# Kernel tuning notes

Hardware: AMD Instinct MI355X
Metric: run time of the kernel (lower is better)

The kernel has to match this reference:

```python
import jax, jax.numpy as jnp
import numpy as np

N = 2_097_152          # sampled points
H = 16                 # hash heads / levels
F = 2                  # features per head
M = 524_288            # 2**19 table size
HID = 64               # mlp width
OUT = 3


def setup_inputs() -> dict:
    key = jax.random.key(0)
    ks = jax.random.split(key, 12)
    idx = jax.random.randint(ks[0], (N, H), 0, M, dtype=jnp.int64)
    tables = jax.random.normal(ks[1], (H, M, F), dtype=jnp.float32) * 0.02
    d_in = H * F  # 32
    def lin(k, d1, d2):
        kw, kb = jax.random.split(k)
        s = 1.0 / np.sqrt(d1)
        W = jax.random.uniform(kw, (d1, d2), jnp.float32, -s, s)
        b = jax.random.uniform(kb, (d2,), jnp.float32, -s, s)
        return W, b
    W1, b1 = lin(ks[2], d_in, HID)
    W2, b2 = lin(ks[3], HID, HID)
    W3, b3 = lin(ks[4], HID, HID)
    W4, b4 = lin(ks[5], HID, OUT)
    return {"idx": idx, "tables": tables,
            "W1": W1, "b1": b1, "W2": W2, "b2": b2,
            "W3": W3, "b3": b3, "W4": W4, "b4": b4}


def reference(idx, tables, W1, b1, W2, b2, W3, b3, W4, b4):
    # per-head gather: tables[h][idx[:, h]] -> [N, H, F], then concat heads
    gather = jax.vmap(lambda t, i: t[i], in_axes=(0, 1), out_axes=1)
    x = gather(tables, idx).reshape(idx.shape[0], -1)  # [N, H*F]
    x = jax.nn.relu(x @ W1 + b1)
    x = jax.nn.relu(x @ W2 + b2)
    x = jax.nn.relu(x @ W3 + b3)
    return x @ W4 + b4  # [N, 3]
```

## Files before the change

kernel.cpp:

```cpp
#include <hip/hip_runtime.h>
#include <hip/hip_bf16.h>

typedef __attribute__((ext_vector_type(8))) short short8;
typedef __attribute__((ext_vector_type(4))) float floatx4;
typedef __attribute__((ext_vector_type(4))) int int4v;
typedef __attribute__((ext_vector_type(4))) unsigned int uint4v;

#define MTBL 524288
#define HSTRIDE 72

union U4S8 { uint4v u; short8 s; };

static __device__ __forceinline__ unsigned int pack2bf(float a, float b) {
    union { float f; unsigned int u; } x, y;
    x.f = a; y.f = b;
    unsigned int lo = (x.u + 0x8000u) >> 16;
    unsigned int hi = (y.u + 0x8000u) & 0xFFFF0000u;
    return lo | hi;
}
static __device__ __forceinline__ short bf1(float a) {
    union { float f; unsigned int u; } x;
    x.f = a;
    return (short)((x.u + 0x8000u) >> 16);
}

__global__ __launch_bounds__(256) void ngp_compress(
    const floatx4* __restrict__ tab4, unsigned int* __restrict__ tblC)
{
    const int t = blockIdx.x * 256 + threadIdx.x;
    floatx4 a = __builtin_nontemporal_load(tab4 + (size_t)2 * t);
    floatx4 b = __builtin_nontemporal_load(tab4 + (size_t)2 * t + 1);
    uint4v w;
    w[0] = pack2bf(a[0], a[1]);
    w[1] = pack2bf(a[2], a[3]);
    w[2] = pack2bf(b[0], b[1]);
    w[3] = pack2bf(b[2], b[3]);
    __builtin_nontemporal_store(w, (uint4v*)(tblC + (size_t)4 * t));
}

__global__ __launch_bounds__(256) void ngp_transpose(
    const int* __restrict__ idx, int* __restrict__ idxT, int N)
{
    const int t  = blockIdx.x * 256 + threadIdx.x;
    const int p0 = t * 4;
    const int4v* rows = (const int4v*)idx;
    int4v r[4][4];
#pragma unroll
    for (int p = 0; p < 4; ++p)
#pragma unroll
        for (int c = 0; c < 4; ++c)
            r[p][c] = __builtin_nontemporal_load(rows + (size_t)(p0 + p) * 4 + c);
#pragma unroll
    for (int c = 0; c < 4; ++c)
#pragma unroll
        for (int k = 0; k < 4; ++k) {
            const int h = c * 4 + k;
            int4v w;
            w[0] = r[0][c][k]; w[1] = r[1][c][k]; w[2] = r[2][c][k]; w[3] = r[3][c][k];
            __builtin_nontemporal_store(w, (int4v*)(idxT + (size_t)h * N + p0));
        }
}

__global__ __launch_bounds__(256) void ngp_gather_ph(
    const int* __restrict__ idxT, const unsigned int* __restrict__ tblC,
    unsigned int* __restrict__ xU, int N, int phase, int iters)
{
    const int h    = ((blockIdx.x & 7) << 1) | phase;
    const int slot = blockIdx.x >> 3;
    const int* __restrict__ ih = idxT + (size_t)h * N;
    const unsigned int* __restrict__ th = tblC + (size_t)h * MTBL;
    unsigned int* __restrict__ xh = xU + (size_t)h * N;

    int p = slot * (N >> 8) + (threadIdx.x << 3);
    int4v iv0 = __builtin_nontemporal_load((const int4v*)(ih + p));
    int4v iv1 = __builtin_nontemporal_load((const int4v*)(ih + p + 4));
    for (int it = 0; it < iters; ++it) {
        int4v nv0, nv1;
        if (it + 1 < iters) {
            nv0 = __builtin_nontemporal_load((const int4v*)(ih + p + 2048));
            nv1 = __builtin_nontemporal_load((const int4v*)(ih + p + 2052));
        }
        uint4v w0, w1;
        w0[0] = th[iv0[0]]; w0[1] = th[iv0[1]]; w0[2] = th[iv0[2]]; w0[3] = th[iv0[3]];
        w1[0] = th[iv1[0]]; w1[1] = th[iv1[1]]; w1[2] = th[iv1[2]]; w1[3] = th[iv1[3]];
        __builtin_nontemporal_store(w0, (uint4v*)(xh + p));
        __builtin_nontemporal_store(w1, (uint4v*)(xh + p + 4));
        iv0 = nv0; iv1 = nv1;
        p += 2048;
    }
}

__global__ __launch_bounds__(256, 2) void ngp_mlp(
    const unsigned int* __restrict__ xU,
    const float* __restrict__ W1, const float* __restrict__ b1,
    const float* __restrict__ W2, const float* __restrict__ b2,
    const float* __restrict__ W3, const float* __restrict__ b3,
    const float* __restrict__ W4, const float* __restrict__ b4,
    float* __restrict__ out, int N, int tiles_per_wave)
{
    __shared__ float sW[6144];
    __shared__ __hip_bfloat16 sH[4][16 * HSTRIDE];

    const int tid  = threadIdx.x;
    const int wave = tid >> 6;
    const int lane = tid & 63;
    const int q = lane >> 4;
    const int m = lane & 15;

    short8 A1[4], A2[4][2], A3[4][2], A4[2];
    floatx4 C1[4], C2[4], C3[4], C4;

    for (int i = tid; i < 2048; i += 256) sW[i] = W1[i];
    for (int i = tid; i < 4096; i += 256) sW[2048 + i] = W2[i];
    __syncthreads();
#pragma unroll
    for (int t = 0; t < 4; ++t) {
        short8 a;
#pragma unroll
        for (int j = 0; j < 8; ++j)
            a[j] = bf1(sW[(q * 8 + j) * 64 + t * 16 + m]);
        A1[t] = a;
    }
#pragma unroll
    for (int t = 0; t < 4; ++t)
#pragma unroll
        for (int c = 0; c < 2; ++c) {
            short8 a;
#pragma unroll
            for (int j = 0; j < 8; ++j)
                a[j] = bf1(sW[2048 + (c * 32 + q * 8 + j) * 64 + t * 16 + m]);
            A2[t][c] = a;
        }
    __syncthreads();

    for (int i = tid; i < 4096; i += 256) sW[i] = W3[i];
    if (tid < 192) sW[4096 + tid] = W4[tid];
    if (tid < 64)       sW[4288 + tid] = b1[tid];
    else if (tid < 128) sW[4288 + tid] = b2[tid - 64];
    else if (tid < 192) sW[4288 + tid] = b3[tid - 128];
    else if (tid < 195) sW[4288 + tid] = b4[tid - 192];
    __syncthreads();
#pragma unroll
    for (int t = 0; t < 4; ++t)
#pragma unroll
        for (int c = 0; c < 2; ++c) {
            short8 a;
#pragma unroll
            for (int j = 0; j < 8; ++j)
                a[j] = bf1(sW[(c * 32 + q * 8 + j) * 64 + t * 16 + m]);
            A3[t][c] = a;
        }
#pragma unroll
    for (int c = 0; c < 2; ++c) {
        short8 a;
#pragma unroll
        for (int j = 0; j < 8; ++j)
            a[j] = (m < 3) ? bf1(sW[4096 + (c * 32 + q * 8 + j) * 3 + m]) : (short)0;
        A4[c] = a;
    }
#pragma unroll
    for (int t = 0; t < 4; ++t)
#pragma unroll
        for (int r = 0; r < 4; ++r) {
            C1[t][r] = sW[4288 + t * 16 + q * 4 + r];
            C2[t][r] = sW[4288 + 64 + t * 16 + q * 4 + r];
            C3[t][r] = sW[4288 + 128 + t * 16 + q * 4 + r];
        }
#pragma unroll
    for (int r = 0; r < 4; ++r)
        C4[r] = (q == 0 && r < 3) ? sW[4288 + 192 + r] : 0.0f;

    __hip_bfloat16* hrow = &sH[wave][m * HSTRIDE];
    const int gw = blockIdx.x * 4 + wave;
    const int tile0 = gw * tiles_per_wave;

    const unsigned int* xr = xU + (size_t)(q * 4) * N + m;

    uint4v cur;
    {
        const int c0 = tile0 * 16;
        cur[0] = xr[c0];
        cur[1] = xr[(size_t)N + c0];
        cur[2] = xr[(size_t)2 * N + c0];
        cur[3] = xr[(size_t)3 * N + c0];
    }

    for (int it = 0; it < tiles_per_wave; ++it) {
        const int pbase = (tile0 + it) * 16;
        const bool more = (it + 1) < tiles_per_wave;

        U4S8 bx; bx.u = cur;
        const short8 Bx = bx.s;

        uint4v nxt;
        if (more) {
            const int cn = pbase + 16;
            nxt[0] = xr[cn];
            nxt[1] = xr[(size_t)N + cn];
            nxt[2] = xr[(size_t)2 * N + cn];
            nxt[3] = xr[(size_t)3 * N + cn];
        }

        floatx4 acc[4];
#pragma unroll
        for (int t = 0; t < 4; ++t)
            acc[t] = __builtin_amdgcn_mfma_f32_16x16x32_bf16(A1[t], Bx, C1[t], 0, 0, 0);

#pragma unroll
        for (int t = 0; t < 4; ++t) {
            uint2 pk;
            pk.x = pack2bf(fmaxf(acc[t][0], 0.f), fmaxf(acc[t][1], 0.f));
            pk.y = pack2bf(fmaxf(acc[t][2], 0.f), fmaxf(acc[t][3], 0.f));
            *(uint2*)(hrow + t * 16 + q * 4) = pk;
        }
        short8 Bh0 = *(const short8*)(hrow + q * 8);
        short8 Bh1 = *(const short8*)(hrow + 32 + q * 8);

#pragma unroll
        for (int t = 0; t < 4; ++t) {
            acc[t] = __builtin_amdgcn_mfma_f32_16x16x32_bf16(A2[t][0], Bh0, C2[t], 0, 0, 0);
            acc[t] = __builtin_amdgcn_mfma_f32_16x16x32_bf16(A2[t][1], Bh1, acc[t], 0, 0, 0);
        }

#pragma unroll
        for (int t = 0; t < 4; ++t) {
            uint2 pk;
            pk.x = pack2bf(fmaxf(acc[t][0], 0.f), fmaxf(acc[t][1], 0.f));
            pk.y = pack2bf(fmaxf(acc[t][2], 0.f), fmaxf(acc[t][3], 0.f));
            *(uint2*)(hrow + t * 16 + q * 4) = pk;
        }
        Bh0 = *(const short8*)(hrow + q * 8);
        Bh1 = *(const short8*)(hrow + 32 + q * 8);

#pragma unroll
        for (int t = 0; t < 4; ++t) {
            acc[t] = __builtin_amdgcn_mfma_f32_16x16x32_bf16(A3[t][0], Bh0, C3[t], 0, 0, 0);
            acc[t] = __builtin_amdgcn_mfma_f32_16x16x32_bf16(A3[t][1], Bh1, acc[t], 0, 0, 0);
        }

#pragma unroll
        for (int t = 0; t < 4; ++t) {
            uint2 pk;
            pk.x = pack2bf(fmaxf(acc[t][0], 0.f), fmaxf(acc[t][1], 0.f));
            pk.y = pack2bf(fmaxf(acc[t][2], 0.f), fmaxf(acc[t][3], 0.f));
            *(uint2*)(hrow + t * 16 + q * 4) = pk;
        }
        Bh0 = *(const short8*)(hrow + q * 8);
        Bh1 = *(const short8*)(hrow + 32 + q * 8);

        floatx4 o;
        o = __builtin_amdgcn_mfma_f32_16x16x32_bf16(A4[0], Bh0, C4, 0, 0, 0);
        o = __builtin_amdgcn_mfma_f32_16x16x32_bf16(A4[1], Bh1, o, 0, 0, 0);

        if (q == 0) {
            const int pn = pbase + m;
            out[pn * 3 + 0] = o[0];
            out[pn * 3 + 1] = o[1];
            out[pn * 3 + 2] = o[2];
        }

        cur = nxt;
    }
}

__global__ __launch_bounds__(256, 2) void ngp_fused(
    const int* __restrict__ idx,
    const float* __restrict__ tables,
    const float* __restrict__ W1, const float* __restrict__ b1,
    const float* __restrict__ W2, const float* __restrict__ b2,
    const float* __restrict__ W3, const float* __restrict__ b3,
    const float* __restrict__ W4, const float* __restrict__ b4,
    float* __restrict__ out, int tiles_per_wave)
{
    __shared__ float sW1[2048];
    __shared__ float sW2[4096];
    __shared__ float sW3[4096];
    __shared__ float sW4[192];
    __shared__ float sB[200];
    __shared__ __hip_bfloat16 sH[4][16 * HSTRIDE];

    const int tid = threadIdx.x;
    for (int i = tid; i < 2048; i += 256) sW1[i] = W1[i];
    for (int i = tid; i < 4096; i += 256) sW2[i] = W2[i];
    for (int i = tid; i < 4096; i += 256) sW3[i] = W3[i];
    if (tid < 192) sW4[tid] = W4[tid];
    if (tid < 64)       sB[tid] = b1[tid];
    else if (tid < 128) sB[tid] = b2[tid - 64];
    else if (tid < 192) sB[tid] = b3[tid - 128];
    else if (tid < 195) sB[tid] = b4[tid - 192];
    __syncthreads();

    const int wave = tid >> 6;
    const int lane = tid & 63;
    const int q = lane >> 4;
    const int m = lane & 15;

    short8 A1[4], A2[4][2], A3[4][2], A4[2];
#pragma unroll
    for (int t = 0; t < 4; ++t) {
        short8 a;
#pragma unroll
        for (int j = 0; j < 8; ++j)
            a[j] = bf1(sW1[(q * 8 + j) * 64 + t * 16 + m]);
        A1[t] = a;
    }
#pragma unroll
    for (int t = 0; t < 4; ++t)
#pragma unroll
        for (int c = 0; c < 2; ++c) {
            short8 a, a3;
#pragma unroll
            for (int j = 0; j < 8; ++j) {
                a[j]  = bf1(sW2[(c * 32 + q * 8 + j) * 64 + t * 16 + m]);
                a3[j] = bf1(sW3[(c * 32 + q * 8 + j) * 64 + t * 16 + m]);
            }
            A2[t][c] = a;
            A3[t][c] = a3;
        }
#pragma unroll
    for (int c = 0; c < 2; ++c) {
        short8 a;
#pragma unroll
        for (int j = 0; j < 8; ++j)
            a[j] = (m < 3) ? bf1(sW4[(c * 32 + q * 8 + j) * 3 + m]) : (short)0;
        A4[c] = a;
    }

    floatx4 C1[4], C2[4], C3[4], C4;
#pragma unroll
    for (int t = 0; t < 4; ++t)
#pragma unroll
        for (int r = 0; r < 4; ++r) {
            C1[t][r] = sB[t * 16 + q * 4 + r];
            C2[t][r] = sB[64 + t * 16 + q * 4 + r];
            C3[t][r] = sB[128 + t * 16 + q * 4 + r];
        }
#pragma unroll
    for (int r = 0; r < 4; ++r)
        C4[r] = (q == 0 && r < 3) ? sB[192 + r] : 0.0f;

    __hip_bfloat16* hrow = &sH[wave][m * HSTRIDE];
    const int4*   idx4 = (const int4*)idx;
    const float2* tbl  = (const float2*)tables;

    const int gw = blockIdx.x * 4 + wave;
    const int tile0 = gw * tiles_per_wave;

    int4 iv = idx4[(tile0 * 16 + m) * 4 + q];
    float2 g0 = tbl[(q * 4 + 0) * MTBL + iv.x];
    float2 g1 = tbl[(q * 4 + 1) * MTBL + iv.y];
    float2 g2 = tbl[(q * 4 + 2) * MTBL + iv.z];
    float2 g3 = tbl[(q * 4 + 3) * MTBL + iv.w];

    for (int it = 0; it < tiles_per_wave; ++it) {
        const int pbase = (tile0 + it) * 16;
        const bool more = (it + 1) < tiles_per_wave;

        short8 Bx;
        {
            unsigned int p0 = pack2bf(g0.x, g0.y);
            unsigned int p1 = pack2bf(g1.x, g1.y);
            unsigned int p2 = pack2bf(g2.x, g2.y);
            unsigned int p3 = pack2bf(g3.x, g3.y);
            Bx[0] = (short)(p0 & 0xFFFF); Bx[1] = (short)(p0 >> 16);
            Bx[2] = (short)(p1 & 0xFFFF); Bx[3] = (short)(p1 >> 16);
            Bx[4] = (short)(p2 & 0xFFFF); Bx[5] = (short)(p2 >> 16);
            Bx[6] = (short)(p3 & 0xFFFF); Bx[7] = (short)(p3 >> 16);
        }

        int4 ivn;
        if (more) ivn = idx4[((pbase + 16) + m) * 4 + q];

        floatx4 acc[4];
#pragma unroll
        for (int t = 0; t < 4; ++t)
            acc[t] = __builtin_amdgcn_mfma_f32_16x16x32_bf16(A1[t], Bx, C1[t], 0, 0, 0);

#pragma unroll
        for (int t = 0; t < 4; ++t) {
            uint2 pk;
            pk.x = pack2bf(fmaxf(acc[t][0], 0.f), fmaxf(acc[t][1], 0.f));
            pk.y = pack2bf(fmaxf(acc[t][2], 0.f), fmaxf(acc[t][3], 0.f));
            *(uint2*)(hrow + t * 16 + q * 4) = pk;
        }
        short8 Bh0 = *(const short8*)(hrow + q * 8);
        short8 Bh1 = *(const short8*)(hrow + 32 + q * 8);

#pragma unroll
        for (int t = 0; t < 4; ++t) {
            acc[t] = __builtin_amdgcn_mfma_f32_16x16x32_bf16(A2[t][0], Bh0, C2[t], 0, 0, 0);
            acc[t] = __builtin_amdgcn_mfma_f32_16x16x32_bf16(A2[t][1], Bh1, acc[t], 0, 0, 0);
        }

        if (more) {
            g0 = tbl[(q * 4 + 0) * MTBL + ivn.x];
            g1 = tbl[(q * 4 + 1) * MTBL + ivn.y];
            g2 = tbl[(q * 4 + 2) * MTBL + ivn.z];
            g3 = tbl[(q * 4 + 3) * MTBL + ivn.w];
        }

#pragma unroll
        for (int t = 0; t < 4; ++t) {
            uint2 pk;
            pk.x = pack2bf(fmaxf(acc[t][0], 0.f), fmaxf(acc[t][1], 0.f));
            pk.y = pack2bf(fmaxf(acc[t][2], 0.f), fmaxf(acc[t][3], 0.f));
            *(uint2*)(hrow + t * 16 + q * 4) = pk;
        }
        Bh0 = *(const short8*)(hrow + q * 8);
        Bh1 = *(const short8*)(hrow + 32 + q * 8);

#pragma unroll
        for (int t = 0; t < 4; ++t) {
            acc[t] = __builtin_amdgcn_mfma_f32_16x16x32_bf16(A3[t][0], Bh0, C3[t], 0, 0, 0);
            acc[t] = __builtin_amdgcn_mfma_f32_16x16x32_bf16(A3[t][1], Bh1, acc[t], 0, 0, 0);
        }

#pragma unroll
        for (int t = 0; t < 4; ++t) {
            uint2 pk;
            pk.x = pack2bf(fmaxf(acc[t][0], 0.f), fmaxf(acc[t][1], 0.f));
            pk.y = pack2bf(fmaxf(acc[t][2], 0.f), fmaxf(acc[t][3], 0.f));
            *(uint2*)(hrow + t * 16 + q * 4) = pk;
        }
        Bh0 = *(const short8*)(hrow + q * 8);
        Bh1 = *(const short8*)(hrow + 32 + q * 8);

        floatx4 o;
        o = __builtin_amdgcn_mfma_f32_16x16x32_bf16(A4[0], Bh0, C4, 0, 0, 0);
        o = __builtin_amdgcn_mfma_f32_16x16x32_bf16(A4[1], Bh1, o, 0, 0, 0);

        if (q == 0) {
            const int pn = pbase + m;
            out[pn * 3 + 0] = o[0];
            out[pn * 3 + 1] = o[1];
            out[pn * 3 + 2] = o[2];
        }
    }
}

extern "C" void kernel_launch(void* const* d_in, const int* in_sizes, int n_in,
                              void* d_out, int out_size, void* d_ws, size_t ws_size,
                              hipStream_t stream) {
    const int*   idx    = (const int*)d_in[0];
    const float* tables = (const float*)d_in[1];
    const float* W1 = (const float*)d_in[2];
    const float* b1 = (const float*)d_in[3];
    const float* W2 = (const float*)d_in[4];
    const float* b2 = (const float*)d_in[5];
    const float* W3 = (const float*)d_in[6];
    const float* b3 = (const float*)d_in[7];
    const float* W4 = (const float*)d_in[8];
    const float* b4 = (const float*)d_in[9];
    float* out = (float*)d_out;

    const int N = in_sizes[0] / 16;
    const int total_tiles = N / 16;

    const size_t idxT_bytes = (size_t)16 * N * 4;
    const size_t xU_bytes   = (size_t)16 * N * 4;
    const size_t tblC_bytes = (size_t)16 * MTBL * 4;
    const size_t need = idxT_bytes + xU_bytes + tblC_bytes;

    if (ws_size >= need) {
        int*          idxT = (int*)d_ws;
        unsigned int* xU   = (unsigned int*)((char*)d_ws + idxT_bytes);
        unsigned int* tblC = (unsigned int*)((char*)d_ws + idxT_bytes + xU_bytes);

        ngp_transpose<<<N / 1024, 256, 0, stream>>>(idx, idxT, N);
        ngp_compress<<<(16 * MTBL) / 1024, 256, 0, stream>>>(
            (const floatx4*)tables, tblC);
        const int iters = (N >> 8) >> 11;
        ngp_gather_ph<<<2048, 256, 0, stream>>>(idxT, tblC, xU, N, 0, iters);
        ngp_gather_ph<<<2048, 256, 0, stream>>>(idxT, tblC, xU, N, 1, iters);
        const int blocks = 2048;
        const int tiles_per_wave = total_tiles / (blocks * 4);
        ngp_mlp<<<blocks, 256, 0, stream>>>(xU, W1, b1, W2, b2, W3, b3, W4, b4,
                                            out, N, tiles_per_wave);
    } else {
        const int blocks = 2048;
        const int tiles_per_wave = total_tiles / (blocks * 4);
        ngp_fused<<<blocks, 256, 0, stream>>>(idx, tables, W1, b1, W2, b2, W3, b3,
                                              W4, b4, out, tiles_per_wave);
    }
}
```

Baseline: 652.5 us.

## Keep MLP activations in registers via permuted weight columns, merge prep kernels

The hidden-layer weight columns and biases are permuted so that the MFMA output layout of one layer matches the B-operand layout the next layer needs. Activations can then be ReLU-packed in registers instead of round-tripping through shared memory. All weights are staged into shared memory in one pass with a single barrier, and the transpose and compress kernels are merged into one launch. This trades larger static shared memory for fewer LDS operations, fewer syncs and one less kernel launch.

```diff
diff --git a/kernel.cpp b/kernel.cpp
--- a/kernel.cpp
+++ b/kernel.cpp
@@ -24,41 +24,50 @@
     return (short)((x.u + 0x8000u) >> 16);
 }
 
-__global__ __launch_bounds__(256) void ngp_compress(
-    const floatx4* __restrict__ tab4, unsigned int* __restrict__ tblC)
+static __device__ __forceinline__ short8 relu_pack(floatx4 a, floatx4 b) {
+    U4S8 r;
+    r.u[0] = pack2bf(fmaxf(a[0], 0.f), fmaxf(a[1], 0.f));
+    r.u[1] = pack2bf(fmaxf(a[2], 0.f), fmaxf(a[3], 0.f));
+    r.u[2] = pack2bf(fmaxf(b[0], 0.f), fmaxf(b[1], 0.f));
+    r.u[3] = pack2bf(fmaxf(b[2], 0.f), fmaxf(b[3], 0.f));
+    return r.s;
+}
+
+__global__ __launch_bounds__(256) void ngp_prep(
+    const int* __restrict__ idx, int* __restrict__ idxT,
+    const floatx4* __restrict__ tab4, unsigned int* __restrict__ tblC, int N)
 {
-    const int t = blockIdx.x * 256 + threadIdx.x;
-    floatx4 a = __builtin_nontemporal_load(tab4 + (size_t)2 * t);
-    floatx4 b = __builtin_nontemporal_load(tab4 + (size_t)2 * t + 1);
-    uint4v w;
-    w[0] = pack2bf(a[0], a[1]);
-    w[1] = pack2bf(a[2], a[3]);
-    w[2] = pack2bf(b[0], b[1]);
-    w[3] = pack2bf(b[2], b[3]);
-    __builtin_nontemporal_store(w, (uint4v*)(tblC + (size_t)4 * t));
-}
-
-__global__ __launch_bounds__(256) void ngp_transpose(
-    const int* __restrict__ idx, int* __restrict__ idxT, int N)
-{
-    const int t  = blockIdx.x * 256 + threadIdx.x;
-    const int p0 = t * 4;
-    const int4v* rows = (const int4v*)idx;
-    int4v r[4][4];
-#pragma unroll
-    for (int p = 0; p < 4; ++p)
+    const int tblocks = N >> 10;
+    if ((int)blockIdx.x < tblocks) {
+        const int t  = blockIdx.x * 256 + threadIdx.x;
+        const int p0 = t * 4;
+        const int4v* rows = (const int4v*)idx;
+        int4v r[4][4];
+#pragma unroll
+        for (int p = 0; p < 4; ++p)
+#pragma unroll
+            for (int c = 0; c < 4; ++c)
+                r[p][c] = __builtin_nontemporal_load(rows + (size_t)(p0 + p) * 4 + c);
 #pragma unroll
         for (int c = 0; c < 4; ++c)
-            r[p][c] = __builtin_nontemporal_load(rows + (size_t)(p0 + p) * 4 + c);
-#pragma unroll
-    for (int c = 0; c < 4; ++c)
-#pragma unroll
-        for (int k = 0; k < 4; ++k) {
-            const int h = c * 4 + k;
-            int4v w;
-            w[0] = r[0][c][k]; w[1] = r[1][c][k]; w[2] = r[2][c][k]; w[3] = r[3][c][k];
-            __builtin_nontemporal_store(w, (int4v*)(idxT + (size_t)h * N + p0));
-        }
+#pragma unroll
+            for (int k = 0; k < 4; ++k) {
+                const int h = c * 4 + k;
+                int4v w;
+                w[0] = r[0][c][k]; w[1] = r[1][c][k]; w[2] = r[2][c][k]; w[3] = r[3][c][k];
+                __builtin_nontemporal_store(w, (int4v*)(idxT + (size_t)h * N + p0));
+            }
+    } else {
+        const int t = (blockIdx.x - tblocks) * 256 + threadIdx.x;
+        floatx4 a = __builtin_nontemporal_load(tab4 + (size_t)2 * t);
+        floatx4 b = __builtin_nontemporal_load(tab4 + (size_t)2 * t + 1);
+        uint4v w;
+        w[0] = pack2bf(a[0], a[1]);
+        w[1] = pack2bf(a[2], a[3]);
+        w[2] = pack2bf(b[0], b[1]);
+        w[3] = pack2bf(b[2], b[3]);
+        __builtin_nontemporal_store(w, (uint4v*)(tblC + (size_t)4 * t));
+    }
 }
 
 __global__ __launch_bounds__(256) void ngp_gather_ph(
@@ -98,79 +107,75 @@
     const float* __restrict__ W4, const float* __restrict__ b4,
     float* __restrict__ out, int N, int tiles_per_wave)
 {
-    __shared__ float sW[6144];
-    __shared__ __hip_bfloat16 sH[4][16 * HSTRIDE];
+    __shared__ float sW[10632];
 
     const int tid  = threadIdx.x;
+    for (int i = tid; i < 2048; i += 256) sW[i] = W1[i];
+    for (int i = tid; i < 4096; i += 256) sW[2048 + i] = W2[i];
+    for (int i = tid; i < 4096; i += 256) sW[6144 + i] = W3[i];
+    if (tid < 192) sW[10240 + tid] = W4[tid];
+    if (tid < 64)       sW[10432 + tid] = b1[tid];
+    else if (tid < 128) sW[10432 + tid] = b2[tid - 64];
+    else if (tid < 192) sW[10432 + tid] = b3[tid - 128];
+    else if (tid < 195) sW[10432 + tid] = b4[tid - 192];
+    __syncthreads();
+
     const int wave = tid >> 6;
     const int lane = tid & 63;
     const int q = lane >> 4;
     const int m = lane & 15;
 
+    int ct[4];
+#pragma unroll
+    for (int t = 0; t < 4; ++t)
+        ct[t] = 32 * (t >> 1) + 4 * (t & 1) + 8 * (m >> 2) + (m & 3);
+
     short8 A1[4], A2[4][2], A3[4][2], A4[2];
     floatx4 C1[4], C2[4], C3[4], C4;
 
-    for (int i = tid; i < 2048; i += 256) sW[i] = W1[i];
-    for (int i = tid; i < 4096; i += 256) sW[2048 + i] = W2[i];
-    __syncthreads();
 #pragma unroll
     for (int t = 0; t < 4; ++t) {
         short8 a;
 #pragma unroll
         for (int j = 0; j < 8; ++j)
-            a[j] = bf1(sW[(q * 8 + j) * 64 + t * 16 + m]);
+            a[j] = bf1(sW[(q * 8 + j) * 64 + ct[t]]);
         A1[t] = a;
     }
 #pragma unroll
     for (int t = 0; t < 4; ++t)
 #pragma unroll
         for (int c = 0; c < 2; ++c) {
-            short8 a;
-#pragma unroll
-            for (int j = 0; j < 8; ++j)
-                a[j] = bf1(sW[2048 + (c * 32 + q * 8 + j) * 64 + t * 16 + m]);
-            A2[t][c] = a;
-        }
-    __syncthreads();
-
-    for (int i = tid; i < 4096; i += 256) sW[i] = W3[i];
-    if (tid < 192) sW[4096 + tid] = W4[tid];
-    if (tid < 64)       sW[4288 + tid] = b1[tid];
-    else if (tid < 128) sW[4288 + tid] = b2[tid - 64];
-    else if (tid < 192) sW[4288 + tid] = b3[tid - 128];
-    else if (tid < 195) sW[4288 + tid] = b4[tid - 192];
-    __syncthreads();
-#pragma unroll
-    for (int t = 0; t < 4; ++t)
-#pragma unroll
-        for (int c = 0; c < 2; ++c) {
-            short8 a;
-#pragma unroll
-            for (int j = 0; j < 8; ++j)
-                a[j] = bf1(sW[(c * 32 + q * 8 + j) * 64 + t * 16 + m]);
-            A3[t][c] = a;
+            short8 a2, a3;
+#pragma unroll
+            for (int j = 0; j < 8; ++j) {
+                a2[j] = bf1(sW[2048 + (c * 32 + q * 8 + j) * 64 + ct[t]]);
+                a3[j] = bf1(sW[6144 + (c * 32 + q * 8 + j) * 64 + ct[t]]);
+            }
+            A2[t][c] = a2;
+            A3[t][c] = a3;
         }
 #pragma unroll
     for (int c = 0; c < 2; ++c) {
         short8 a;
 #pragma unroll
         for (int j = 0; j < 8; ++j)
-            a[j] = (m < 3) ? bf1(sW[4096 + (c * 32 + q * 8 + j) * 3 + m]) : (short)0;
+            a[j] = (m < 3) ? bf1(sW[10240 + (c * 32 + q * 8 + j) * 3 + m]) : (short)0;
         A4[c] = a;
     }
 #pragma unroll
-    for (int t = 0; t < 4; ++t)
+    for (int t = 0; t < 4; ++t) {
+        const int bi = 32 * (t >> 1) + 4 * (t & 1) + 8 * q;
 #pragma unroll
         for (int r = 0; r < 4; ++r) {
-            C1[t][r] = sW[4288 + t * 16 + q * 4 + r];
-            C2[t][r] = sW[4288 + 64 + t * 16 + q * 4 + r];
-            C3[t][r] = sW[4288 + 128 + t * 16 + q * 4 + r];
-        }
+            C1[t][r] = sW[10432 + bi + r];
+            C2[t][r] = sW[10432 + 64 + bi + r];
+            C3[t][r] = sW[10432 + 128 + bi + r];
+        }
+    }
 #pragma unroll
     for (int r = 0; r < 4; ++r)
-        C4[r] = (q == 0 && r < 3) ? sW[4288 + 192 + r] : 0.0f;
-
-    __hip_bfloat16* hrow = &sH[wave][m * HSTRIDE];
+        C4[r] = (q == 0 && r < 3) ? sW[10432 + 192 + r] : 0.0f;
+
     const int gw = blockIdx.x * 4 + wave;
     const int tile0 = gw * tiles_per_wave;
 
@@ -201,56 +206,35 @@
             nxt[3] = xr[(size_t)3 * N + cn];
         }
 
-        floatx4 acc[4];
+        floatx4 h1[4];
 #pragma unroll
         for (int t = 0; t < 4; ++t)
-            acc[t] = __builtin_amdgcn_mfma_f32_16x16x32_bf16(A1[t], Bx, C1[t], 0, 0, 0);
-
-#pragma unroll
-        for (int t = 0; t < 4; ++t) {
-            uint2 pk;
-            pk.x = pack2bf(fmaxf(acc[t][0], 0.f), fmaxf(acc[t][1], 0.f));
-            pk.y = pack2bf(fmaxf(acc[t][2], 0.f), fmaxf(acc[t][3], 0.f));
-            *(uint2*)(hrow + t * 16 + q * 4) = pk;
-        }
-        short8 Bh0 = *(const short8*)(hrow + q * 8);
-        short8 Bh1 = *(const short8*)(hrow + 32 + q * 8);
-
-#pragma unroll
-        for (int t = 0; t < 4; ++t) {
-            acc[t] = __builtin_amdgcn_mfma_f32_16x16x32_bf16(A2[t][0], Bh0, C2[t], 0, 0, 0);
-            acc[t] = __builtin_amdgcn_mfma_f32_16x16x32_bf16(A2[t][1], Bh1, acc[t], 0, 0, 0);
-        }
-
-#pragma unroll
-        for (int t = 0; t < 4; ++t) {
-            uint2 pk;
-            pk.x = pack2bf(fmaxf(acc[t][0], 0.f), fmaxf(acc[t][1], 0.f));
-            pk.y = pack2bf(fmaxf(acc[t][2], 0.f), fmaxf(acc[t][3], 0.f));
-            *(uint2*)(hrow + t * 16 + q * 4) = pk;
-        }
-        Bh0 = *(const short8*)(hrow + q * 8);
-        Bh1 = *(const short8*)(hrow + 32 + q * 8);
-
-#pragma unroll
-        for (int t = 0; t < 4; ++t) {
-            acc[t] = __builtin_amdgcn_mfma_f32_16x16x32_bf16(A3[t][0], Bh0, C3[t], 0, 0, 0);
-            acc[t] = __builtin_amdgcn_mfma_f32_16x16x32_bf16(A3[t][1], Bh1, acc[t], 0, 0, 0);
-        }
-
-#pragma unroll
-        for (int t = 0; t < 4; ++t) {
-            uint2 pk;
-            pk.x = pack2bf(fmaxf(acc[t][0], 0.f), fmaxf(acc[t][1], 0.f));
-            pk.y = pack2bf(fmaxf(acc[t][2], 0.f), fmaxf(acc[t][3], 0.f));
-            *(uint2*)(hrow + t * 16 + q * 4) = pk;
-        }
-        Bh0 = *(const short8*)(hrow + q * 8);
-        Bh1 = *(const short8*)(hrow + 32 + q * 8);
+            h1[t] = __builtin_amdgcn_mfma_f32_16x16x32_bf16(A1[t], Bx, C1[t], 0, 0, 0);
+
+        short8 B0 = relu_pack(h1[0], h1[1]);
+        short8 B1 = relu_pack(h1[2], h1[3]);
+
+        floatx4 h2[4];
+#pragma unroll
+        for (int t = 0; t < 4; ++t) {
+            h2[t] = __builtin_amdgcn_mfma_f32_16x16x32_bf16(A2[t][0], B0, C2[t], 0, 0, 0);
+            h2[t] = __builtin_amdgcn_mfma_f32_16x16x32_bf16(A2[t][1], B1, h2[t], 0, 0, 0);
+        }
+        B0 = relu_pack(h2[0], h2[1]);
+        B1 = relu_pack(h2[2], h2[3]);
+
+        floatx4 h3[4];
+#pragma unroll
+        for (int t = 0; t < 4; ++t) {
+            h3[t] = __builtin_amdgcn_mfma_f32_16x16x32_bf16(A3[t][0], B0, C3[t], 0, 0, 0);
+            h3[t] = __builtin_amdgcn_mfma_f32_16x16x32_bf16(A3[t][1], B1, h3[t], 0, 0, 0);
+        }
+        B0 = relu_pack(h3[0], h3[1]);
+        B1 = relu_pack(h3[2], h3[3]);
 
         floatx4 o;
-        o = __builtin_amdgcn_mfma_f32_16x16x32_bf16(A4[0], Bh0, C4, 0, 0, 0);
-        o = __builtin_amdgcn_mfma_f32_16x16x32_bf16(A4[1], Bh1, o, 0, 0, 0);
+        o = __builtin_amdgcn_mfma_f32_16x16x32_bf16(A4[0], B0, C4, 0, 0, 0);
+        o = __builtin_amdgcn_mfma_f32_16x16x32_bf16(A4[1], B1, o, 0, 0, 0);
 
         if (q == 0) {
             const int pn = pbase + m;
@@ -466,9 +450,10 @@
         unsigned int* xU   = (unsigned int*)((char*)d_ws + idxT_bytes);
         unsigned int* tblC = (unsigned int*)((char*)d_ws + idxT_bytes + xU_bytes);
 
-        ngp_transpose<<<N / 1024, 256, 0, stream>>>(idx, idxT, N);
-        ngp_compress<<<(16 * MTBL) / 1024, 256, 0, stream>>>(
-            (const floatx4*)tables, tblC);
+        const int tblocks = N / 1024;
+        const int cblocks = (16 * MTBL) / 1024;
+        ngp_prep<<<tblocks + cblocks, 256, 0, stream>>>(
+            idx, idxT, (const floatx4*)tables, tblC, N);
         const int iters = (N >> 8) >> 11;
         ngp_gather_ph<<<2048, 256, 0, stream>>>(idxT, tblC, xU, N, 0, iters);
         ngp_gather_ph<<<2048, 256, 0, stream>>>(idxT, tblC, xU, N, 1, iters);
```

New measurement: 632.4 us. 3.1% less time.
